# Performance work log

Hardware: AMD Instinct MI355X
Metric: run time of the kernel (lower is better)

## Reference

```python
import jax, jax.numpy as jnp
import numpy as np

DIM = 1024
H = 16
HKV = 4
HD = DIM // H  # 64
GROUP = H // HKV
ROPE_BASE = 10000.0
B, T = 2, 2048


def rms_norm(x, eps):
    return x * jax.lax.rsqrt(jnp.mean(x * x, axis=-1, keepdims=True) + eps)


def apply_rotary(x, cos, sin):
    # x: [B, h, T, HD]; cos/sin: [1, 1, T, HD//2]
    half = x.shape[-1] // 2
    x1, x2 = x[..., :half], x[..., half:]
    return jnp.concatenate([x1 * cos + x2 * sin, -x1 * sin + x2 * cos], axis=-1)


def setup_inputs() -> dict:
    key = jax.random.key(0)
    ks = jax.random.split(key, 5)
    s = 0.02
    return {
        "x": jax.random.normal(ks[0], (B, T, DIM), dtype=jnp.float32),
        "Wq": jax.random.normal(ks[1], (DIM, DIM), dtype=jnp.float32) * s,
        "Wk": jax.random.normal(ks[2], (HKV * HD, DIM), dtype=jnp.float32) * s,
        "Wv": jax.random.normal(ks[3], (HKV * HD, DIM), dtype=jnp.float32) * s,
        "Wproj": jax.random.normal(ks[4], (DIM, DIM), dtype=jnp.float32) * s,
        "q_gain": jnp.full((H,), 12.0, dtype=jnp.float32),
    }


def reference(x, Wq, Wk, Wv, Wproj, q_gain):
    bsz, seqlen, dim = x.shape
    eps = jnp.asarray(jnp.finfo(x.dtype).eps, x.dtype)

    # double RMSNorm path: normalized input for q/k, raw input for v
    x_qk = rms_norm(x, eps)
    q = (x_qk @ Wq.T).reshape(bsz, seqlen, H, HD).transpose(0, 2, 1, 3)    # [B,H,T,D]
    k = (x_qk @ Wk.T).reshape(bsz, seqlen, HKV, HD).transpose(0, 2, 1, 3)  # [B,Hkv,T,D]
    v = (x @ Wv.T).reshape(bsz, seqlen, HKV, HD).transpose(0, 2, 1, 3)     # [B,Hkv,T,D]

    q = rms_norm(q, eps)
    k = rms_norm(k, eps)

    # rotary embeddings
    t = jnp.arange(seqlen, dtype=jnp.float32)
    inv_freq = 1.0 / (ROPE_BASE ** (jnp.arange(0, HD, 2, dtype=jnp.float32) / HD))
    freqs = jnp.outer(t, inv_freq)                       # [T, HD//2]
    cos = jnp.cos(freqs)[None, None].astype(x.dtype)
    sin = jnp.sin(freqs)[None, None].astype(x.dtype)
    q = apply_rotary(q, cos, sin)
    k = apply_rotary(k, cos, sin)

    # per-head gain on q
    q = q * q_gain.astype(q.dtype)[None, :, None, None]

    # GQA: expand kv heads to query heads
    k_r = jnp.repeat(k, GROUP, axis=1)  # [B,H,T,D]
    v_r = jnp.repeat(v, GROUP, axis=1)

    scale = 1.0 / np.sqrt(HD)
    scores = jnp.einsum("bhqd,bhkd->bhqk", q, k_r) * scale
    causal = jnp.tril(jnp.ones((seqlen, seqlen), dtype=bool))
    scores = jnp.where(causal[None, None], scores, jnp.asarray(-jnp.inf, scores.dtype))
    attn = jax.nn.softmax(scores, axis=-1)
    y = jnp.einsum("bhqk,bhkd->bhqd", attn, v_r)          # [B,H,T,D]

    # XSA: remove value-direction component from output
    y_bt = y.transpose(0, 2, 1, 3)                        # [B,T,H,D]
    v_bt = v.transpose(0, 2, 1, 3)                        # [B,T,Hkv,D]
    y_g = y_bt.reshape(bsz, seqlen, HKV, GROUP, HD)
    vnorm = jnp.sqrt(jnp.sum(v_bt * v_bt, axis=-1, keepdims=True))
    vn = (v_bt / jnp.maximum(vnorm, 1e-12))[..., None, :]  # [B,T,Hkv,1,D]
    proj = jnp.sum(y_g * vn, axis=-1, keepdims=True) * vn
    y_bt = (y_g - proj).reshape(bsz, seqlen, H, HD)

    return y_bt.reshape(bsz, seqlen, dim) @ Wproj.T
```

## Files before the change

### kernel.cpp

```cpp
#include <hip/hip_runtime.h>
#include <hip/hip_bf16.h>

typedef __attribute__((ext_vector_type(8))) short bf8v;
typedef __attribute__((ext_vector_type(4))) float f4v;

#define MFMA16(a,b,c) __builtin_amdgcn_mfma_f32_16x16x32_bf16((a),(b),(c),0,0,0)

#define GLD16(gp, lp) __builtin_amdgcn_global_load_lds( \
    (const __attribute__((address_space(1))) void*)(gp), \
    (__attribute__((address_space(3))) void*)(lp), 16, 0, 0)

#define DIMC   1024
#define TSEQ   2048
#define NH     16
#define NKV    4
#define HDIM   64
#define RMS_EPS 1.1920929e-07f
#define QSCALE 0.1803368801111601f

__device__ __forceinline__ ushort f2bf(float f) {
  unsigned u = __builtin_bit_cast(unsigned, f);
  u = (u + 0x7FFFu + ((u >> 16) & 1u)) >> 16;
  return (ushort)u;
}
__device__ __forceinline__ float bf2f(ushort u) {
  return __builtin_bit_cast(float, (unsigned)u << 16);
}
__device__ __forceinline__ unsigned cvtpk(float lo, float hi) {
  unsigned r;
  asm("v_cvt_pk_bf16_f32 %0, %1, %2" : "=v"(r) : "v"(lo), "v"(hi));
  return r;
}

__global__ __launch_bounds__(256) void prep_all(
    const float* __restrict__ x,
    const float* __restrict__ Wq, const float* __restrict__ Wk,
    const float* __restrict__ Wv, const float* __restrict__ Wp,
    ushort* __restrict__ xhi, ushort* __restrict__ xlo,
    ushort* __restrict__ xb,
    ushort* __restrict__ wqkh, ushort* __restrict__ wqkl,
    ushort* __restrict__ wvb, ushort* __restrict__ wpb,
    float* __restrict__ cosT, float* __restrict__ sinT) {
  __shared__ float red[4];
  int bid = blockIdx.x, tid = threadIdx.x;
  if (bid < 4096) {
    int row = bid;
    int lane = tid & 63, w = tid >> 6;
    float4 v = ((const float4*)(x + (size_t)row * DIMC))[tid];
    float ss = v.x * v.x + v.y * v.y + v.z * v.z + v.w * v.w;
    for (int off = 32; off; off >>= 1) ss += __shfl_xor(ss, off);
    if (lane == 0) red[w] = ss;
    __syncthreads();
    float tot = red[0] + red[1] + red[2] + red[3];
    float rs = rsqrtf(tot * (1.0f / DIMC) + RMS_EPS);
    float n0 = v.x * rs, n1 = v.y * rs, n2 = v.z * rs, n3 = v.w * rs;
    ushort4 h, l, ob;
    h.x = f2bf(n0); l.x = f2bf(n0 - bf2f(h.x));
    h.y = f2bf(n1); l.y = f2bf(n1 - bf2f(h.y));
    h.z = f2bf(n2); l.z = f2bf(n2 - bf2f(h.z));
    h.w = f2bf(n3); l.w = f2bf(n3 - bf2f(h.w));
    ob.x = f2bf(v.x); ob.y = f2bf(v.y); ob.z = f2bf(v.z); ob.w = f2bf(v.w);
    ((ushort4*)(xhi + (size_t)row * DIMC))[tid] = h;
    ((ushort4*)(xlo + (size_t)row * DIMC))[tid] = l;
    ((ushort4*)(xb  + (size_t)row * DIMC))[tid] = ob;
    return;
  }
  int wb = bid - 4096;
  if (wb < 1280) {
    const float* src;
    size_t si, di;
    if (wb < 1024) { src = Wq; si = (size_t)wb * 256 + tid; di = si; }
    else { src = Wk; si = (size_t)(wb - 1024) * 256 + tid; di = 262144 + si; }
    float4 v = ((const float4*)src)[si];
    ushort4 h, l;
    h.x = f2bf(v.x); l.x = f2bf(v.x - bf2f(h.x));
    h.y = f2bf(v.y); l.y = f2bf(v.y - bf2f(h.y));
    h.z = f2bf(v.z); l.z = f2bf(v.z - bf2f(h.z));
    h.w = f2bf(v.w); l.w = f2bf(v.w - bf2f(h.w));
    ((ushort4*)wqkh)[di] = h;
    ((ushort4*)wqkl)[di] = l;
  } else if (wb < 2560) {
    const float* src;
    ushort* dst;
    int i;
    if (wb < 1536) { src = Wv; dst = wvb; i = (wb - 1280) * 256 + tid; }
    else           { src = Wp; dst = wpb; i = (wb - 1536) * 256 + tid; }
    float4 v = ((const float4*)src)[i];
    ushort4 o;
    o.x = f2bf(v.x); o.y = f2bf(v.y); o.z = f2bf(v.z); o.w = f2bf(v.w);
    ((ushort4*)dst)[i] = o;
  } else {
    int i = (wb - 2560) * 256 + tid;
    int t = i >> 5, j = i & 31;
    float inv = 1.0f / powf(10000.0f, (float)j * (1.0f / 32.0f));
    float f = (float)t * inv;
    cosT[i] = cosf(f);
    sinT[i] = sinf(f);
  }
}

__global__ __launch_bounds__(256, 3)
void gemm_qkv(const ushort* __restrict__ xhi, const ushort* __restrict__ xlo,
              const ushort* __restrict__ wqkh, const ushort* __restrict__ wqkl,
              float* __restrict__ QKf, ushort* __restrict__ QKc,
              const ushort* __restrict__ xb, const ushort* __restrict__ wvb,
              float* __restrict__ Vf) {
  __shared__ __align__(16) ushort lA[128 * 64];
  __shared__ __align__(16) ushort lB[128 * 64];
  const int bid = blockIdx.x;
  int u;
  bool big;
  if (bid < 256)      { big = true;  u = bid; }
  else if (bid < 448) { big = false; u = bid - 256; }
  else if (bid < 512) { big = true;  u = 256 + (bid - 448); }
  else                { big = false; u = 192 + (bid - 512); }

  const ushort *Ap0, *Bp0, *Ap1, *Bp1;
  float* Cf = QKf;
  int N = 1280, nsteps, mt, n0;
  if (big) {
    mt = u / 10; n0 = (u % 10) * 128;
    Ap0 = xlo; Bp0 = wqkh; Ap1 = xhi; Bp1 = wqkl; nsteps = 32;
  } else if (u < 320) {
    mt = u / 10; n0 = (u % 10) * 128;
    Ap0 = xhi; Bp0 = wqkh; Ap1 = Ap0; Bp1 = Bp0; nsteps = 16;
  } else {
    int v = u - 320; mt = v >> 1; n0 = (v & 1) * 128;
    Ap0 = xb; Bp0 = wvb; Ap1 = Ap0; Bp1 = Bp0; nsteps = 16;
    Cf = Vf; N = 256;
  }
  const int m0 = mt * 128;

  const int t = threadIdx.x;
  const int lane = t & 63, w = t >> 6;
  const int wr = w >> 1, wc = w & 1;
  const int l15 = lane & 15, lg = lane >> 4;
  const int srow = t >> 3, scp = t & 7;

  f4v acc[4][4] = {};

  for (int s = 0; s < nsteps; ++s) {
    const ushort* Ab = (s < 16) ? Ap0 : Ap1;
    const ushort* Bb = (s < 16) ? Bp0 : Bp1;
    const int kk = (s & 15) * 64;
    for (int i = 0; i < 4; ++i) {
      int row = srow + i * 32;
      int sc = scp ^ (row & 7);
      const ushort* ga = Ab + (size_t)(m0 + row) * DIMC + kk + sc * 8;
      const ushort* gb = Bb + (size_t)(n0 + row) * DIMC + kk + sc * 8;
      GLD16(ga, &lA[w * 512 + i * 2048]);
      GLD16(gb, &lB[w * 512 + i * 2048]);
    }
    __syncthreads();
    for (int kx = 0; kx < 2; ++kx) {
      bf8v af[4], bfr[4];
      for (int m = 0; m < 4; ++m) {
        int row = wr * 64 + m * 16 + l15;
        int ch = (kx * 4 + lg) ^ (row & 7);
        af[m] = *(const bf8v*)&lA[row * 64 + ch * 8];
      }
      for (int n = 0; n < 4; ++n) {
        int row = wc * 64 + n * 16 + l15;
        int ch = (kx * 4 + lg) ^ (row & 7);
        bfr[n] = *(const bf8v*)&lB[row * 64 + ch * 8];
      }
      for (int m = 0; m < 4; ++m)
        for (int n = 0; n < 4; ++n)
          acc[m][n] = MFMA16(af[m], bfr[n], acc[m][n]);
    }
    __syncthreads();
  }

  if (big) {
    for (int m = 0; m < 4; ++m)
      for (int n = 0; n < 4; ++n)
        for (int j = 0; j < 4; ++j) {
          int r = m0 + wr * 64 + m * 16 + lg * 4 + j;
          int c = n0 + wc * 64 + n * 16 + l15;
          QKc[(size_t)r * 1280 + c] = f2bf(acc[m][n][j]);
        }
  } else {
    for (int m = 0; m < 4; ++m)
      for (int n = 0; n < 4; ++n)
        for (int j = 0; j < 4; ++j) {
          int r = m0 + wr * 64 + m * 16 + lg * 4 + j;
          int c = n0 + wc * 64 + n * 16 + l15;
          Cf[(size_t)r * N + c] = acc[m][n][j];
        }
  }
}

__global__ __launch_bounds__(256, 2)
void gemm_bt(const ushort* __restrict__ A0, const ushort* __restrict__ B0,
             float* __restrict__ C, int N) {
  __shared__ __align__(16) ushort lA[128 * 64];
  __shared__ __align__(16) ushort lB[128 * 64];
  const int t = threadIdx.x;
  const int lane = t & 63, w = t >> 6;
  const int wr = w >> 1, wc = w & 1;
  const int l15 = lane & 15, lg = lane >> 4;
  const int m0 = blockIdx.y * 128, n0 = blockIdx.x * 128;
  const int srow = t >> 3, scp = t & 7;

  f4v acc[4][4] = {};

  for (int k0 = 0; k0 < 1024; k0 += 64) {
    for (int i = 0; i < 4; ++i) {
      int row = srow + i * 32;
      int sc = scp ^ (row & 7);
      const ushort* ga = A0 + (size_t)(m0 + row) * DIMC + k0 + sc * 8;
      const ushort* gb = B0 + (size_t)(n0 + row) * DIMC + k0 + sc * 8;
      GLD16(ga, &lA[w * 512 + i * 2048]);
      GLD16(gb, &lB[w * 512 + i * 2048]);
    }
    __syncthreads();
    for (int kx = 0; kx < 2; ++kx) {
      bf8v af[4], bfr[4];
      for (int m = 0; m < 4; ++m) {
        int row = wr * 64 + m * 16 + l15;
        int ch = (kx * 4 + lg) ^ (row & 7);
        af[m] = *(const bf8v*)&lA[row * 64 + ch * 8];
      }
      for (int n = 0; n < 4; ++n) {
        int row = wc * 64 + n * 16 + l15;
        int ch = (kx * 4 + lg) ^ (row & 7);
        bfr[n] = *(const bf8v*)&lB[row * 64 + ch * 8];
      }
      for (int m = 0; m < 4; ++m)
        for (int n = 0; n < 4; ++n)
          acc[m][n] = MFMA16(af[m], bfr[n], acc[m][n]);
    }
    __syncthreads();
  }

  for (int m = 0; m < 4; ++m)
    for (int n = 0; n < 4; ++n)
      for (int j = 0; j < 4; ++j) {
        int r = m0 + wr * 64 + m * 16 + lg * 4 + j;
        int c = n0 + wc * 64 + n * 16 + l15;
        C[(size_t)r * N + c] = acc[m][n][j];
      }
}

__global__ __launch_bounds__(256) void post_all(
    const float* __restrict__ QKf, const ushort* __restrict__ QKc,
    const float* __restrict__ cosT,
    const float* __restrict__ sinT, const float* __restrict__ qgain,
    ushort* __restrict__ qhi, ushort* __restrict__ qlo,
    ushort* __restrict__ kb16,
    const float* __restrict__ Vf, ushort* __restrict__ vt2,
    ushort* __restrict__ vhat_t) {
  __shared__ float lds[64][69];
  __shared__ float rnv[64];
  int bid = blockIdx.x;
  if (bid < 4096) {
    int m = bid;
    int b = m >> 11, tpos = m & 2047;
    int lane = threadIdx.x & 63, w = threadIdx.x >> 6;
    int d = lane, j = d & 31;
    float sgn = (d < 32) ? 1.0f : -1.0f;
    float c = cosT[tpos * 32 + j], s = sinT[tpos * 32 + j];

    for (int i = 0; i < 4; ++i) {
      int h = w * 4 + i;
      size_t base = (size_t)m * 1280 + h * HDIM + d;
      float q = QKf[base] + bf2f(QKc[base]);
      float ss = q * q;
      for (int off = 32; off; off >>= 1) ss += __shfl_xor(ss, off);
      float rs = rsqrtf(ss * (1.0f / HDIM) + RMS_EPS);
      float qn = q * rs;
      float partner = __shfl_xor(qn, 32);
      float ro = (qn * c + sgn * partner * s) * (qgain[h] * QSCALE);
      ushort hi = f2bf(ro);
      ushort lo = f2bf(ro - bf2f(hi));
      size_t idx = (((size_t)b * NH + h) * TSEQ + tpos) * HDIM + d;
      qhi[idx] = hi;
      qlo[idx] = lo;
    }
    {
      int kv = w;
      size_t base = (size_t)m * 1280 + 1024 + kv * HDIM + d;
      float k = QKf[base] + bf2f(QKc[base]);
      float ss = k * k;
      for (int off = 32; off; off >>= 1) ss += __shfl_xor(ss, off);
      float rs = rsqrtf(ss * (1.0f / HDIM) + RMS_EPS);
      float kn = k * rs;
      float partner = __shfl_xor(kn, 32);
      float ro = kn * c + sgn * partner * s;
      kb16[((size_t)(b * NKV + kv) * TSEQ + tpos) * HDIM + d] = f2bf(ro);
    }
    return;
  }
  {
    int vb = bid - 4096;
    int bkv = vb >> 5, tt = vb & 31;
    int b = bkv >> 2, kv = bkv & 3;
    int tid = threadIdx.x;
    for (int i = 0; i < 16; ++i) {
      int idx = i * 256 + tid;
      int tloc = idx >> 6, d = idx & 63;
      lds[d][tloc] = Vf[((size_t)(b * TSEQ + tt * 64 + tloc)) * 256 + kv * 64 + d];
    }
    __syncthreads();
    {
      int t = tid >> 2, prt = tid & 3;
      float ssum = 0.f;
      for (int dd = 0; dd < 16; ++dd) {
        float v = lds[prt * 16 + dd][t];
        ssum += v * v;
      }
      ssum += __shfl_xor(ssum, 1);
      ssum += __shfl_xor(ssum, 2);
      if (prt == 0) rnv[t] = 1.0f / fmaxf(sqrtf(ssum), 1e-12f);
    }
    __syncthreads();
    for (int i = 0; i < 16; ++i) {
      int idx = i * 256 + tid;
      int d = idx >> 6, tloc = idx & 63;
      float v = lds[d][tloc];
      vt2[(size_t)bkv * (TSEQ * 64) + tt * 4096 + d * 64 + tloc] = f2bf(v);
      vhat_t[(size_t)bkv * (TSEQ * 64) + (size_t)d * TSEQ + tt * 64 + tloc] = f2bf(v * rnv[tloc]);
    }
  }
}

__global__ __launch_bounds__(128, 2) void attn_kern(
    const ushort* __restrict__ qhi, const ushort* __restrict__ qlo,
    const ushort* __restrict__ kb16, const ushort* __restrict__ vt2,
    const ushort* __restrict__ vhat_t, ushort* __restrict__ ytil) {
  __shared__ __align__(16) ushort lk[2][64 * 64];
  __shared__ __align__(16) ushort lv[2][64 * 64];
  const int t = threadIdx.x;
  const int lane = t & 63, w = t >> 6;
  const int bid = blockIdx.x;
  const int xcd = bid & 7, g = (bid >> 3) & 3, rank = bid >> 5;
  const int tile32 = 63 - rank;
  const int b = xcd >> 2, kv = xcd & 3, h = kv * 4 + g;
  const int l15 = lane & 15, lg = lane >> 4;
  const int q0 = tile32 * 32 + w * 16;
  const int ntile = (tile32 >> 1) + 1;
  const int t3 = t >> 3, tc8 = t & 7;
  const int rx = l15 & 7;
  const int pswz = rx << 2;

  const size_t qoff = (((size_t)(b * NH + h)) * TSEQ + q0 + l15) * HDIM;
  bf8v bq0h = *(const bf8v*)(qhi + qoff + lg * 8);
  bf8v bq1h = *(const bf8v*)(qhi + qoff + 32 + lg * 8);
  bf8v bq0l = *(const bf8v*)(qlo + qoff + lg * 8);
  bf8v bq1l = *(const bf8v*)(qlo + qoff + 32 + lg * 8);

  const ushort* kb = kb16 + (size_t)(b * NKV + kv) * TSEQ * 64;
  const ushort* vb = vt2 + (size_t)(b * NKV + kv) * TSEQ * 64;

#define STAGE(BUF, IT) do { \
    _Pragma("unroll") \
    for (int i = 0; i < 4; ++i) { \
      int row = i * 16 + t3; \
      int sc = tc8 ^ (row & 7); \
      GLD16(kb + (size_t)((IT) * 64 + row) * 64 + sc * 8, \
            &lk[BUF][(i * 16 + (w << 3)) * 64]); \
      GLD16(vb + (size_t)(IT) * 4096 + row * 64 + sc * 8, \
            &lv[BUF][(i * 16 + (w << 3)) * 64]); \
    } } while (0)

  STAGE(0, 0);

  f4v y[4] = {};
  float mrow = -1e30f, lrow = 0.f;

#pragma unroll 1
  for (int it = 0; it < ntile; ++it) {
    const int cur = it & 1;
    __syncthreads();
    if (it + 1 < ntile) STAGE(cur ^ 1, it + 1);

    const ushort* lkc = &lk[cur][0];
    const ushort* lvc = &lv[cur][0];
    unsigned* pw = (unsigned*)&lk[cur][w << 10];
    const int kv0 = it * 64;

    f4v s[4];
    __builtin_amdgcn_s_setprio(1);
#pragma unroll
    for (int n = 0; n < 4; ++n) {
      const ushort* krow = lkc + (n * 16 + l15) * 64;
      bf8v kh0 = *(const bf8v*)&krow[((0 + lg) ^ rx) * 8];
      bf8v kh1 = *(const bf8v*)&krow[((4 + lg) ^ rx) * 8];
      f4v z = {};
      f4v acc = MFMA16(kh0, bq0h, z);
      acc = MFMA16(kh1, bq1h, acc);
      acc = MFMA16(kh0, bq0l, acc);
      acc = MFMA16(kh1, bq1l, acc);
      s[n] = acc;
    }
    __builtin_amdgcn_s_setprio(0);

    const bool need_mask = (it == ntile - 1);
    float mloc = -1e30f;
#pragma unroll
    for (int n = 0; n < 4; ++n)
#pragma unroll
      for (int j = 0; j < 4; ++j) {
        float v = s[n][j];
        if (need_mask && (kv0 + n * 16 + lg * 4 + j > q0 + l15)) v = -1e30f;
        s[n][j] = v;
        mloc = fmaxf(mloc, v);
      }
    if (__any(mloc > mrow + 11.5f)) {
      float mf = fmaxf(mloc, __shfl_xor(mloc, 16));
      mf = fmaxf(mf, __shfl_xor(mf, 32));
      float mnew = fmaxf(mrow, mf);
      float scf = exp2f(mrow - mnew);
      lrow *= scf;
#pragma unroll
      for (int n = 0; n < 4; ++n) y[n] *= scf;
      mrow = mnew;
    }
#pragma unroll
    for (int n = 0; n < 4; ++n)
#pragma unroll
      for (int j = 0; j < 4; ++j) {
        float e = exp2f(s[n][j] - mrow);
        s[n][j] = e;
        lrow += e;
      }

    asm volatile("s_waitcnt lgkmcnt(0)" ::: "memory");
    __builtin_amdgcn_s_barrier();

#pragma unroll
    for (int n = 0; n < 4; ++n) {
      uint2 pk;
      pk.x = cvtpk(s[n][0], s[n][1]);
      pk.y = cvtpk(s[n][2], s[n][3]);
      *(uint2*)&pw[l15 * 32 + ((8 * n + 2 * lg) ^ pswz)] = pk;
    }
    asm volatile("s_waitcnt lgkmcnt(0)" ::: "memory");
    bf8v pb0 = *(const bf8v*)&pw[l15 * 32 + ((lg * 4) ^ pswz)];
    bf8v pb1 = *(const bf8v*)&pw[l15 * 32 + ((16 + lg * 4) ^ pswz)];
    __builtin_amdgcn_s_setprio(1);
#pragma unroll
    for (int n = 0; n < 4; ++n) {
      const ushort* vrow = lvc + (n * 16 + l15) * 64;
      bf8v va0 = *(const bf8v*)&vrow[((0 + lg) ^ rx) * 8];
      bf8v va1 = *(const bf8v*)&vrow[((4 + lg) ^ rx) * 8];
      y[n] = MFMA16(va0, pb0, y[n]);
      y[n] = MFMA16(va1, pb1, y[n]);
    }
    __builtin_amdgcn_s_setprio(0);
  }
#undef STAGE

  {
    lrow += __shfl_xor(lrow, 16);
    lrow += __shfl_xor(lrow, 32);
    float inv = 1.0f / lrow;
    const int lastcur = (ntile - 1) & 1;
    ushort* yw = (ushort*)&lk[lastcur][w << 10];
    const ushort* vh = vhat_t + (size_t)(b * NKV + kv) * TSEQ * 64;
    float vv[4][4];
    float dp = 0.f;
#pragma unroll
    for (int n = 0; n < 4; ++n)
#pragma unroll
      for (int j = 0; j < 4; ++j) {
        int d = n * 16 + lg * 4 + j;
        float yv = y[n][j] * inv;
        y[n][j] = yv;
        vv[n][j] = bf2f(vh[(size_t)d * TSEQ + q0 + l15]);
        dp += yv * vv[n][j];
      }
    dp += __shfl_xor(dp, 16);
    dp += __shfl_xor(dp, 32);
#pragma unroll
    for (int n = 0; n < 4; ++n)
#pragma unroll
      for (int j = 0; j < 4; ++j) {
        int d = n * 16 + lg * 4 + j;
        yw[l15 * 64 + (((d >> 3) ^ rx) << 3) + (d & 7)] = f2bf(y[n][j] - dp * vv[n][j]);
      }
    asm volatile("s_waitcnt lgkmcnt(0)" ::: "memory");
    int row = lane >> 2, quad = lane & 3;
    bf8v y0 = *(const bf8v*)(yw + row * 64 + ((quad ^ (row & 7)) << 3));
    bf8v y1 = *(const bf8v*)(yw + row * 64 + (((quad + 4) ^ (row & 7)) << 3));
    size_t gbase = ((size_t)(b * TSEQ + q0 + row)) * DIMC + h * HDIM + quad * 8;
    *(bf8v*)(ytil + gbase) = y0;
    *(bf8v*)(ytil + gbase + 32) = y1;
  }
}

extern "C" void kernel_launch(void* const* d_in, const int* in_sizes, int n_in,
                              void* d_out, int out_size, void* d_ws, size_t ws_size,
                              hipStream_t stream) {
  (void)in_sizes; (void)n_in; (void)out_size; (void)ws_size;
  const float* x  = (const float*)d_in[0];
  const float* Wq = (const float*)d_in[1];
  const float* Wk = (const float*)d_in[2];
  const float* Wv = (const float*)d_in[3];
  const float* Wp = (const float*)d_in[4];
  const float* qg = (const float*)d_in[5];
  float* out = (float*)d_out;
  char* ws = (char*)d_ws;
  const size_t KB = 1024, MB = 1ull << 20;

  ushort* xhi = (ushort*)(ws);
  ushort* xlo = (ushort*)(ws + 8 * MB);
  ushort* xb  = (ushort*)(ws + 16 * MB);
  ushort* wqkh = (ushort*)(ws + 24 * MB);
  ushort* wqkl = (ushort*)(ws + 26 * MB + 512 * KB);
  ushort* wvb = (ushort*)(ws + 29 * MB);
  ushort* wpb = (ushort*)(ws + 29 * MB + 512 * KB);
  float*  cosT = (float*)(ws + 31 * MB + 512 * KB);
  float*  sinT = (float*)(ws + 31 * MB + 768 * KB);
  float*  QKf  = (float*)(ws + 32 * MB);
  ushort* kb16 = (ushort*)(ws + 52 * MB);
  ushort* vt2  = (ushort*)(ws + 54 * MB);
  ushort* vhat = (ushort*)(ws + 56 * MB);

  float*  Vf   = out;
  ushort* QKc  = (ushort*)((char*)out + 4 * MB);
  ushort* qhb  = xhi;
  ushort* qlb  = xlo;
  ushort* ytil = xb;

  prep_all<<<6912, 256, 0, stream>>>(x, Wq, Wk, Wv, Wp, xhi, xlo, xb,
                                     wqkh, wqkl, wvb, wpb, cosT, sinT);

  gemm_qkv<<<704, 256, 0, stream>>>(xhi, xlo, wqkh, wqkl, QKf, QKc,
                                    xb, wvb, Vf);

  post_all<<<4352, 256, 0, stream>>>(QKf, QKc, cosT, sinT, qg, qhb, qlb, kb16,
                                     Vf, vt2, vhat);
  attn_kern<<<2048, 128, 0, stream>>>(qhb, qlb, kb16, vt2, vhat, ytil);
  gemm_bt<<<dim3(8, 32), 256, 0, stream>>>(ytil, wpb, out, 1024);
}
```

Measured before the change: 155.1 us.

## Split causal attention into KV chunks with a separate combine and XSA kernel

```diff
diff --git a/kernel.cpp b/kernel.cpp
--- a/kernel.cpp
+++ b/kernel.cpp
@@ -249,7 +249,7 @@
     ushort* __restrict__ qhi, ushort* __restrict__ qlo,
     ushort* __restrict__ kb16,
     const float* __restrict__ Vf, ushort* __restrict__ vt2,
-    ushort* __restrict__ vhat_t) {
+    ushort* __restrict__ vhat_q) {
   __shared__ float lds[64][69];
   __shared__ float rnv[64];
   int bid = blockIdx.x;
@@ -317,28 +317,42 @@
     for (int i = 0; i < 16; ++i) {
       int idx = i * 256 + tid;
       int d = idx >> 6, tloc = idx & 63;
-      float v = lds[d][tloc];
-      vt2[(size_t)bkv * (TSEQ * 64) + tt * 4096 + d * 64 + tloc] = f2bf(v);
-      vhat_t[(size_t)bkv * (TSEQ * 64) + (size_t)d * TSEQ + tt * 64 + tloc] = f2bf(v * rnv[tloc]);
-    }
-  }
-}
-
-__global__ __launch_bounds__(128, 2) void attn_kern(
+      vt2[(size_t)bkv * (TSEQ * 64) + tt * 4096 + d * 64 + tloc] = f2bf(lds[d][tloc]);
+    }
+    for (int i = 0; i < 16; ++i) {
+      int idx = i * 256 + tid;
+      int tloc = idx >> 6, d = idx & 63;
+      vhat_q[((size_t)bkv * TSEQ + tt * 64 + tloc) * 64 + d] =
+          f2bf(lds[d][tloc] * rnv[tloc]);
+    }
+  }
+}
+
+__global__ __launch_bounds__(256, 4) void attn_chunk(
     const ushort* __restrict__ qhi, const ushort* __restrict__ qlo,
     const ushort* __restrict__ kb16, const ushort* __restrict__ vt2,
-    const ushort* __restrict__ vhat_t, ushort* __restrict__ ytil) {
+    ushort* __restrict__ pyb, float* __restrict__ pml) {
   __shared__ __align__(16) ushort lk[2][64 * 64];
   __shared__ __align__(16) ushort lv[2][64 * 64];
+  __shared__ __align__(16) unsigned pl[4][512];
   const int t = threadIdx.x;
   const int lane = t & 63, w = t >> 6;
   const int bid = blockIdx.x;
-  const int xcd = bid & 7, g = (bid >> 3) & 3, rank = bid >> 5;
-  const int tile32 = 63 - rank;
+  const int combo = bid & 31;
+  const int s = 59 - (bid >> 5);
+  int tile, ci;
+  if (s < 12)      { tile = s; ci = 0; }
+  else if (s < 36) { tile = 12 + ((s - 12) >> 1); ci = (s - 12) & 1; }
+  else             { int z = s - 36; tile = 24 + z / 3; ci = z % 3; }
+  const int nch = (tile <= 11) ? 1 : (tile <= 23 ? 2 : 3);
+  const int ktot = tile + 1, base = ktot / nch, rem = ktot % nch;
+  const int kb0 = ci * base + (ci < rem ? ci : rem);
+  const int len = base + (ci < rem ? 1 : 0);
+
+  const int xcd = combo & 7, g = (combo >> 3) & 3;
   const int b = xcd >> 2, kv = xcd & 3, h = kv * 4 + g;
   const int l15 = lane & 15, lg = lane >> 4;
-  const int q0 = tile32 * 32 + w * 16;
-  const int ntile = (tile32 >> 1) + 1;
+  const int q0 = tile * 64 + w * 16;
   const int t3 = t >> 3, tc8 = t & 7;
   const int rx = l15 & 7;
   const int pswz = rx << 2;
@@ -351,35 +365,36 @@
 
   const ushort* kb = kb16 + (size_t)(b * NKV + kv) * TSEQ * 64;
   const ushort* vb = vt2 + (size_t)(b * NKV + kv) * TSEQ * 64;
-
-#define STAGE(BUF, IT) do { \
+  unsigned* pw = &pl[w][0];
+
+#define STAGE(BUF, KT) do { \
     _Pragma("unroll") \
-    for (int i = 0; i < 4; ++i) { \
-      int row = i * 16 + t3; \
+    for (int i = 0; i < 2; ++i) { \
+      int row = i * 32 + t3; \
       int sc = tc8 ^ (row & 7); \
-      GLD16(kb + (size_t)((IT) * 64 + row) * 64 + sc * 8, \
-            &lk[BUF][(i * 16 + (w << 3)) * 64]); \
-      GLD16(vb + (size_t)(IT) * 4096 + row * 64 + sc * 8, \
-            &lv[BUF][(i * 16 + (w << 3)) * 64]); \
+      GLD16(kb + (size_t)((KT) * 64 + row) * 64 + sc * 8, \
+            &lk[BUF][(i * 32 + (w << 3)) * 64]); \
+      GLD16(vb + (size_t)(KT) * 4096 + row * 64 + sc * 8, \
+            &lv[BUF][(i * 32 + (w << 3)) * 64]); \
     } } while (0)
 
-  STAGE(0, 0);
+  STAGE(0, kb0);
 
   f4v y[4] = {};
   float mrow = -1e30f, lrow = 0.f;
 
 #pragma unroll 1
-  for (int it = 0; it < ntile; ++it) {
-    const int cur = it & 1;
-    __syncthreads();
-    if (it + 1 < ntile) STAGE(cur ^ 1, it + 1);
+  for (int itc = 0; itc < len; ++itc) {
+    const int cur = itc & 1;
+    const int kt = kb0 + itc;
+    __syncthreads();
+    if (itc + 1 < len) STAGE(cur ^ 1, kt + 1);
 
     const ushort* lkc = &lk[cur][0];
     const ushort* lvc = &lv[cur][0];
-    unsigned* pw = (unsigned*)&lk[cur][w << 10];
-    const int kv0 = it * 64;
-
-    f4v s[4];
+    const int kv0 = kt * 64;
+
+    f4v s4[4];
     __builtin_amdgcn_s_setprio(1);
 #pragma unroll
     for (int n = 0; n < 4; ++n) {
@@ -391,19 +406,19 @@
       acc = MFMA16(kh1, bq1h, acc);
       acc = MFMA16(kh0, bq0l, acc);
       acc = MFMA16(kh1, bq1l, acc);
-      s[n] = acc;
+      s4[n] = acc;
     }
     __builtin_amdgcn_s_setprio(0);
 
-    const bool need_mask = (it == ntile - 1);
+    const bool need_mask = (kt == tile);
     float mloc = -1e30f;
 #pragma unroll
     for (int n = 0; n < 4; ++n)
 #pragma unroll
       for (int j = 0; j < 4; ++j) {
-        float v = s[n][j];
+        float v = s4[n][j];
         if (need_mask && (kv0 + n * 16 + lg * 4 + j > q0 + l15)) v = -1e30f;
-        s[n][j] = v;
+        s4[n][j] = v;
         mloc = fmaxf(mloc, v);
       }
     if (__any(mloc > mrow + 11.5f)) {
@@ -420,19 +435,16 @@
     for (int n = 0; n < 4; ++n)
 #pragma unroll
       for (int j = 0; j < 4; ++j) {
-        float e = exp2f(s[n][j] - mrow);
-        s[n][j] = e;
+        float e = exp2f(s4[n][j] - mrow);
+        s4[n][j] = e;
         lrow += e;
       }
-
-    asm volatile("s_waitcnt lgkmcnt(0)" ::: "memory");
-    __builtin_amdgcn_s_barrier();
 
 #pragma unroll
     for (int n = 0; n < 4; ++n) {
       uint2 pk;
-      pk.x = cvtpk(s[n][0], s[n][1]);
-      pk.y = cvtpk(s[n][2], s[n][3]);
+      pk.x = cvtpk(s4[n][0], s4[n][1]);
+      pk.y = cvtpk(s4[n][2], s4[n][3]);
       *(uint2*)&pw[l15 * 32 + ((8 * n + 2 * lg) ^ pswz)] = pk;
     }
     asm volatile("s_waitcnt lgkmcnt(0)" ::: "memory");
@@ -454,39 +466,93 @@
   {
     lrow += __shfl_xor(lrow, 16);
     lrow += __shfl_xor(lrow, 32);
-    float inv = 1.0f / lrow;
-    const int lastcur = (ntile - 1) & 1;
-    ushort* yw = (ushort*)&lk[lastcur][w << 10];
-    const ushort* vh = vhat_t + (size_t)(b * NKV + kv) * TSEQ * 64;
-    float vv[4][4];
-    float dp = 0.f;
-#pragma unroll
-    for (int n = 0; n < 4; ++n)
-#pragma unroll
-      for (int j = 0; j < 4; ++j) {
-        int d = n * 16 + lg * 4 + j;
-        float yv = y[n][j] * inv;
-        y[n][j] = yv;
-        vv[n][j] = bf2f(vh[(size_t)d * TSEQ + q0 + l15]);
-        dp += yv * vv[n][j];
-      }
-    dp += __shfl_xor(dp, 16);
-    dp += __shfl_xor(dp, 32);
-#pragma unroll
-    for (int n = 0; n < 4; ++n)
-#pragma unroll
-      for (int j = 0; j < 4; ++j) {
-        int d = n * 16 + lg * 4 + j;
-        yw[l15 * 64 + (((d >> 3) ^ rx) << 3) + (d & 7)] = f2bf(y[n][j] - dp * vv[n][j]);
-      }
-    asm volatile("s_waitcnt lgkmcnt(0)" ::: "memory");
-    int row = lane >> 2, quad = lane & 3;
-    bf8v y0 = *(const bf8v*)(yw + row * 64 + ((quad ^ (row & 7)) << 3));
-    bf8v y1 = *(const bf8v*)(yw + row * 64 + (((quad + 4) ^ (row & 7)) << 3));
-    size_t gbase = ((size_t)(b * TSEQ + q0 + row)) * DIMC + h * HDIM + quad * 8;
-    *(bf8v*)(ytil + gbase) = y0;
-    *(bf8v*)(ytil + gbase + 32) = y1;
-  }
+    const int slot = combo * 60 + s;
+    ushort* pb = pyb + (size_t)slot * 4096;
+    const int q = w * 16 + l15;
+#pragma unroll
+    for (int n = 0; n < 4; ++n) {
+      uint2 pk;
+      pk.x = cvtpk(y[n][0], y[n][1]);
+      pk.y = cvtpk(y[n][2], y[n][3]);
+      *(uint2*)&pb[q * 64 + n * 16 + lg * 4] = pk;
+    }
+    if (lane < 16) {
+      float* mlp = pml + (size_t)slot * 128;
+      mlp[q] = mrow;
+      mlp[64 + q] = lrow;
+    }
+  }
+}
+
+__global__ __launch_bounds__(256) void combine_kern(
+    const ushort* __restrict__ pyb, const float* __restrict__ pml,
+    const ushort* __restrict__ vhat_q, ushort* __restrict__ ytil) {
+  const int bid = blockIdx.x;
+  const int combo = bid & 31, tile = bid >> 5;
+  const int xcd = combo & 7, g = (combo >> 3) & 3;
+  const int b = xcd >> 2, kv = xcd & 3, h = kv * 4 + g;
+  const int nch = (tile <= 11) ? 1 : (tile <= 23 ? 2 : 3);
+  const int sb = (tile <= 11) ? tile
+               : (tile <= 23) ? 12 + 2 * (tile - 12)
+                              : 36 + 3 * (tile - 24);
+  const int tid = threadIdx.x;
+  const int q = tid >> 2, ds = (tid & 3) * 16;
+  const int q0 = tile * 64;
+
+  float m[3], l[3];
+#pragma unroll
+  for (int ci = 0; ci < 3; ++ci) {
+    if (ci < nch) {
+      const float* mlp = pml + (size_t)(combo * 60 + sb + ci) * 128;
+      m[ci] = mlp[q];
+      l[ci] = mlp[64 + q];
+    } else { m[ci] = -1e30f; l[ci] = 0.f; }
+  }
+  float M = fmaxf(m[0], fmaxf(m[1], m[2]));
+  float y[16] = {};
+  float ltot = 0.f;
+#pragma unroll
+  for (int ci = 0; ci < 3; ++ci) {
+    if (ci < nch) {
+      float sc = exp2f(m[ci] - M);
+      ltot += l[ci] * sc;
+      const ushort* pb = pyb + (size_t)(combo * 60 + sb + ci) * 4096 + q * 64 + ds;
+      bf8v p0 = *(const bf8v*)pb;
+      bf8v p1 = *(const bf8v*)(pb + 8);
+#pragma unroll
+      for (int dd = 0; dd < 8; ++dd) {
+        y[dd] += sc * bf2f((ushort)p0[dd]);
+        y[8 + dd] += sc * bf2f((ushort)p1[dd]);
+      }
+    }
+  }
+  float inv = 1.0f / ltot;
+  const ushort* vh = vhat_q + ((size_t)(b * NKV + kv) * TSEQ + q0 + q) * 64 + ds;
+  bf8v v0 = *(const bf8v*)vh;
+  bf8v v1 = *(const bf8v*)(vh + 8);
+  float vv[16];
+  float dp = 0.f;
+#pragma unroll
+  for (int dd = 0; dd < 8; ++dd) {
+    vv[dd] = bf2f((ushort)v0[dd]);
+    vv[8 + dd] = bf2f((ushort)v1[dd]);
+  }
+#pragma unroll
+  for (int dd = 0; dd < 16; ++dd) {
+    y[dd] *= inv;
+    dp += y[dd] * vv[dd];
+  }
+  dp += __shfl_xor(dp, 1);
+  dp += __shfl_xor(dp, 2);
+  bf8v o0, o1;
+#pragma unroll
+  for (int dd = 0; dd < 8; ++dd) {
+    o0[dd] = (short)f2bf(y[dd] - dp * vv[dd]);
+    o1[dd] = (short)f2bf(y[8 + dd] - dp * vv[8 + dd]);
+  }
+  ushort* yo = ytil + ((size_t)(b * TSEQ + q0 + q)) * DIMC + h * HDIM + ds;
+  *(bf8v*)yo = o0;
+  *(bf8v*)(yo + 8) = o1;
 }
 
 extern "C" void kernel_launch(void* const* d_in, const int* in_sizes, int n_in,
@@ -515,13 +581,15 @@
   float*  QKf  = (float*)(ws + 32 * MB);
   ushort* kb16 = (ushort*)(ws + 52 * MB);
   ushort* vt2  = (ushort*)(ws + 54 * MB);
-  ushort* vhat = (ushort*)(ws + 56 * MB);
 
   float*  Vf   = out;
   ushort* QKc  = (ushort*)((char*)out + 4 * MB);
+  ushort* vhat_q = (ushort*)((char*)out + 14 * MB);
   ushort* qhb  = xhi;
   ushort* qlb  = xlo;
   ushort* ytil = xb;
+  ushort* pyb = (ushort*)(ws + 32 * MB);
+  float*  pml = (float*)(ws + 48 * MB);
 
   prep_all<<<6912, 256, 0, stream>>>(x, Wq, Wk, Wv, Wp, xhi, xlo, xb,
                                      wqkh, wqkl, wvb, wpb, cosT, sinT);
@@ -530,7 +598,8 @@
                                     xb, wvb, Vf);
 
   post_all<<<4352, 256, 0, stream>>>(QKf, QKc, cosT, sinT, qg, qhb, qlb, kb16,
-                                     Vf, vt2, vhat);
-  attn_kern<<<2048, 128, 0, stream>>>(qhb, qlb, kb16, vt2, vhat, ytil);
+                                     Vf, vt2, vhat_q);
+  attn_chunk<<<1920, 256, 0, stream>>>(qhb, qlb, kb16, vt2, pyb, pml);
+  combine_kern<<<1024, 256, 0, stream>>>(pyb, pml, vhat_q, ytil);
   gemm_bt<<<dim3(8, 32), 256, 0, stream>>>(ytil, wpb, out, 1024);
 }
```

Result: faster. 146.5 us (-5.6%).
